# Optimization experiments

Hardware: AMD Instinct MI355X
Metric: run time of the kernel (lower is better)

## Reference

```python
import math
import jax, jax.numpy as jnp
import numpy as np

N_HEAD = 16

def rms_norm(x, w, eps=1e-6):
    x32 = x.astype(jnp.float32)
    ms = jnp.mean(x32 * x32, axis=-1, keepdims=True)
    y = (x32 * jax.lax.rsqrt(ms + eps)).astype(x.dtype)
    return y * w

def apply_rope(x, cos, sin):
    # x: [B,H,S,D], cos/sin: [S,D/2] broadcast over B,H
    half = x.shape[-1] // 2
    x1, x2 = x[..., :half], x[..., half:]
    return jnp.concatenate((x1 * cos - x2 * sin, x2 * cos + x1 * sin), axis=-1).astype(x.dtype)

def setup_inputs() -> dict:
    key = jax.random.key(0)
    ks = jax.random.split(key, 8)
    B, S, D = 1, 4096, 1024
    hd = D // N_HEAD
    x = jax.random.normal(ks[0], (B, S, D), dtype=jnp.float32)
    # rotary embeddings
    inv_freq = 1.0 / (10000.0 ** (jnp.arange(0, hd, 2, dtype=jnp.float32) / hd))  # [hd/2]
    ang = jnp.arange(S, dtype=jnp.float32)[:, None] * inv_freq  # [S, hd/2]
    cos, sin = jnp.cos(ang), jnp.sin(ang)
    # additive causal mask [1,1,S,S]
    causal = jnp.tril(jnp.ones((S, S), dtype=bool))
    attention_mask = jnp.where(causal, 0.0, -1e9).astype(jnp.float32)[None, None]
    init = 0.02
    wq = jax.random.normal(ks[1], (D, D), dtype=jnp.float32) * init
    wk = jax.random.normal(ks[2], (D, D), dtype=jnp.float32) * init
    wv = jax.random.normal(ks[3], (D, D), dtype=jnp.float32) * init
    wo = jax.random.normal(ks[4], (D, D), dtype=jnp.float32) * init
    q_norm_w = jnp.ones((hd,), dtype=jnp.float32)
    k_norm_w = jnp.ones((hd,), dtype=jnp.float32)
    return {"x": x, "cos": cos, "sin": sin, "attention_mask": attention_mask,
            "wq": wq, "wk": wk, "wv": wv, "wo": wo,
            "q_norm_w": q_norm_w, "k_norm_w": k_norm_w}

def reference(x, cos, sin, attention_mask, wq, wk, wv, wo, q_norm_w, k_norm_w):
    B, S, D = x.shape
    H = N_HEAD
    hd = D // H
    q = (x @ wq.T).reshape(B, S, H, hd)
    k = (x @ wk.T).reshape(B, S, H, hd)
    v = (x @ wv.T).reshape(B, S, H, hd)
    q = jnp.swapaxes(rms_norm(q, q_norm_w), 1, 2)  # [B,H,S,hd]
    k = jnp.swapaxes(rms_norm(k, k_norm_w), 1, 2)
    v = jnp.swapaxes(v, 1, 2)
    q = apply_rope(q, cos, sin)
    k = apply_rope(k, cos, sin)
    scores = jnp.einsum('bhqd,bhkd->bhqk', q, k) / math.sqrt(hd)
    scores = scores + attention_mask
    attn = jax.nn.softmax(scores.astype(jnp.float32), axis=-1).astype(q.dtype)
    o = jnp.einsum('bhqk,bhkd->bhqd', attn, v)  # [B,H,S,hd]
    o = jnp.swapaxes(o, 1, 2).reshape(B, S, D)
    return o @ wo.T
```

## Files before the change

### kernel.cpp

```cpp
#include <hip/hip_runtime.h>

#define S_LEN 4096
#define DIM   1024
#define NH    16
#define HD    64

typedef __bf16 bf16;
typedef __attribute__((ext_vector_type(8)))  __bf16 bf16x8;
typedef __attribute__((ext_vector_type(4)))  float  f32x4;
typedef __attribute__((ext_vector_type(16))) float  f32x16;
typedef __attribute__((ext_vector_type(4)))  unsigned int uint4v;

typedef __attribute__((address_space(3))) void lds_void;
typedef __attribute__((address_space(1))) void g_void;

#if __has_builtin(__builtin_amdgcn_exp2f)
#define EXP2(x) __builtin_amdgcn_exp2f(x)
#else
#define EXP2(x) exp2f(x)
#endif

__device__ __forceinline__ void gl_lds16(const void* g, void* l) {
    __builtin_amdgcn_global_load_lds((g_void*)(void*)g, (lds_void*)l, 16, 0, 0);
}

__device__ __forceinline__ unsigned int pk2(float a, float b) {
    unsigned short ua = __builtin_bit_cast(unsigned short, (bf16)a);
    unsigned short ub = __builtin_bit_cast(unsigned short, (bf16)b);
    return (unsigned int)ua | ((unsigned int)ub << 16);
}

__device__ __forceinline__ int ksw23(int x) {
    return (x & ~12) | ((x & 8) >> 1) | ((x & 4) << 1);
}

__global__ __launch_bounds__(256) void f2b_all(
    const float* __restrict__ x,  const float* __restrict__ wq,
    const float* __restrict__ wk, const float* __restrict__ wv,
    const float* __restrict__ wo,
    bf16* __restrict__ xb, bf16* __restrict__ wqkv, bf16* __restrict__ wob)
{
    int b = blockIdx.x;
    const float* src; bf16* dst; int base;
    if (b < 2048)      { src = x;  dst = xb;              base = b; }
    else if (b < 2560) { src = wq; dst = wqkv;            base = b - 2048; }
    else if (b < 3072) { src = wk; dst = wqkv + 1048576;  base = b - 2560; }
    else if (b < 3584) { src = wv; dst = wqkv + 2097152;  base = b - 3072; }
    else               { src = wo; dst = wob;             base = b - 3584; }
    int i = base * 2048 + threadIdx.x * 8;
    float4 a = *(const float4*)(src + i);
    float4 c = *(const float4*)(src + i + 4);
    bf16x8 r;
    r[0]=(bf16)a.x; r[1]=(bf16)a.y; r[2]=(bf16)a.z; r[3]=(bf16)a.w;
    r[4]=(bf16)c.x; r[5]=(bf16)c.y; r[6]=(bf16)c.z; r[7]=(bf16)c.w;
    *(bf16x8*)(dst + i) = r;
}

template <int MODE>
__global__ __launch_bounds__(256) void gemm_bt(
    const bf16* __restrict__ A, const bf16* __restrict__ B,
    int M, int N, int K,
    float* __restrict__ outF,
    bf16* __restrict__ outQ, bf16* __restrict__ outK, bf16* __restrict__ outV,
    const float* __restrict__ cosb, const float* __restrict__ sinb,
    const float* __restrict__ qw,   const float* __restrict__ kw)
{
    __shared__ bf16 As[128][32];
    __shared__ bf16 Bs[128][32];
    const int bm = blockIdx.x, bn = blockIdx.y;
    const int tid  = threadIdx.x;
    const int wave = tid >> 6, lane = tid & 63;
    const int g = lane >> 4, r = lane & 15;
    const int wr = wave >> 1, wc = wave & 1;
    const int rr = lane >> 2, cc = (lane & 3) * 8;

    f32x4 acc[4][4] = {};

    const bf16* Ab = A + (size_t)(bm * 128) * K;
    const bf16* Bb = B + (size_t)(bn * 128) * K;

    for (int k0 = 0; k0 < K; k0 += 32) {
        #pragma unroll
        for (int i = 0; i < 2; ++i) {
            gl_lds16(Ab + (size_t)(wave*32 + i*16 + rr) * K + k0 + cc, &As[wave*32 + i*16][0]);
            gl_lds16(Bb + (size_t)(wave*32 + i*16 + rr) * K + k0 + cc, &Bs[wave*32 + i*16][0]);
        }
        __syncthreads();
        bf16x8 a[4], b[4];
        #pragma unroll
        for (int m = 0; m < 4; ++m) a[m] = *(const bf16x8*)&As[wr*64 + m*16 + r][g*8];
        #pragma unroll
        for (int n = 0; n < 4; ++n) b[n] = *(const bf16x8*)&Bs[wc*64 + n*16 + r][g*8];
        #pragma unroll
        for (int m = 0; m < 4; ++m)
            #pragma unroll
            for (int n = 0; n < 4; ++n)
                acc[m][n] = __builtin_amdgcn_mfma_f32_16x16x32_bf16(a[m], b[n], acc[m][n], 0, 0, 0);
        __syncthreads();
    }

    if (MODE == 0) {
        #pragma unroll
        for (int m = 0; m < 4; ++m)
            #pragma unroll
            for (int n = 0; n < 4; ++n)
                #pragma unroll
                for (int i = 0; i < 4; ++i) {
                    int row = bm*128 + wr*64 + m*16 + g*4 + i;
                    int col = bn*128 + wc*64 + n*16 + r;
                    outF[(size_t)row * N + col] = acc[m][n][i];
                }
    } else if (bn >= 16) {
        #pragma unroll
        for (int m = 0; m < 4; ++m)
            #pragma unroll
            for (int n = 0; n < 4; ++n)
                #pragma unroll
                for (int i = 0; i < 4; ++i) {
                    int row = bm*128 + wr*64 + m*16 + g*4 + i;
                    int col = bn*128 + wc*64 + n*16 + r;
                    int c2 = col - 2048;
                    int hh = c2 >> 6, d = c2 & 63;
                    int pos = ksw23(row & 63) ^ ((d & 7) << 3);
                    outV[((size_t)(hh * HD + d)) * S_LEN + (row & ~63) + pos] = (bf16)acc[m][n][i];
                }
    } else {
        const bool isK = (bn >= 8);
        const float* wn = isK ? kw : qw;
        bf16* dst = isK ? outK : outQ;
        const int h = ((bn & 7) << 1) | wc;
        float wv4[4];
        #pragma unroll
        for (int n = 0; n < 4; ++n) wv4[n] = wn[n * 16 + r];
        #pragma unroll
        for (int m = 0; m < 4; ++m)
            #pragma unroll
            for (int i = 0; i < 4; ++i) {
                int srow = bm*128 + wr*64 + m*16 + g*4 + i;
                float ss = acc[m][0][i]*acc[m][0][i] + acc[m][1][i]*acc[m][1][i]
                         + acc[m][2][i]*acc[m][2][i] + acc[m][3][i]*acc[m][3][i];
                ss += __shfl_xor(ss, 1);
                ss += __shfl_xor(ss, 2);
                ss += __shfl_xor(ss, 4);
                ss += __shfl_xor(ss, 8);
                float rn = rsqrtf(ss * (1.0f / 64.0f) + 1e-6f);
                float xn0 = acc[m][0][i] * rn * wv4[0];
                float xn1 = acc[m][1][i] * rn * wv4[1];
                float xn2 = acc[m][2][i] * rn * wv4[2];
                float xn3 = acc[m][3][i] * rn * wv4[3];
                float c0 = cosb[srow * 32 + r],      c1 = cosb[srow * 32 + 16 + r];
                float s0 = sinb[srow * 32 + r],      s1 = sinb[srow * 32 + 16 + r];
                float y0 = xn0 * c0 - xn2 * s0;
                float y1 = xn1 * c1 - xn3 * s1;
                float y2 = xn2 * c0 + xn0 * s0;
                float y3 = xn3 * c1 + xn1 * s1;
                size_t ob = ((size_t)h * S_LEN + srow) * HD;
                if (isK) {
                    int sw = (srow & 7) << 3;
                    dst[ob + ((     r) ^ sw)] = (bf16)y0;
                    dst[ob + ((16 + r) ^ sw)] = (bf16)y1;
                    dst[ob + ((32 + r) ^ sw)] = (bf16)y2;
                    dst[ob + ((48 + r) ^ sw)] = (bf16)y3;
                } else {
                    dst[ob +      r] = (bf16)y0;
                    dst[ob + 16 + r] = (bf16)y1;
                    dst[ob + 32 + r] = (bf16)y2;
                    dst[ob + 48 + r] = (bf16)y3;
                }
            }
    }
}

__global__ __launch_bounds__(256, 4) void attn_kernel(
    const bf16* __restrict__ q, const bf16* __restrict__ k,
    const bf16* __restrict__ vt,
    bf16* __restrict__ Opc, float* __restrict__ lpc)
{
    __shared__ bf16 Ks[2][64][64];
    __shared__ bf16 Vt[2][64][64];

    const int idx = blockIdx.x;
    const int h = idx & 15;
    const int u = idx >> 4;
    const int qt = 31 - (u >> 2);
    const int c  = u & 3;
    const int nt = 2 * qt + 2;
    const int t0 = (c * nt) >> 2;
    const int t1 = ((c + 1) * nt) >> 2;

    const int q0 = qt * 128;
    const int tid = threadIdx.x;
    const int wave = tid >> 6, lane = tid & 63;
    const int l31 = lane & 31, hi = lane >> 5;

    const bf16* qh  = q  + (size_t)h * S_LEN * HD;
    const bf16* kh  = k  + (size_t)h * S_LEN * HD;
    const bf16* vth = vt + (size_t)h * HD * S_LEN;

    const int qrow = q0 + wave * 32 + l31;
    bf16x8 qf[4];
    #pragma unroll
    for (int ds4 = 0; ds4 < 4; ++ds4)
        qf[ds4] = *(const bf16x8*)(qh + (size_t)qrow * HD + ds4 * 16 + hi * 8);

    float l_run = 0.f;
    f32x16 acc_o[2] = {};

    const int srow = lane >> 3, scol = (lane & 7) * 8;
    const float C1 = 0.125f * 1.44269504088896f;
    const float C2 = 8.0f * 1.44269504088896f;

    auto stage = [&](int t, int buf) {
        const int k0 = t * 64;
        const bf16* kb = kh + (size_t)(k0 + wave * 16) * HD;
        gl_lds16(kb + (size_t)(srow    ) * HD + scol, &Ks[buf][wave * 16][0]);
        gl_lds16(kb + (size_t)(srow + 8) * HD + scol, &Ks[buf][wave * 16 + 8][0]);
        const bf16* vb = vth + (size_t)(wave * 16) * S_LEN + k0;
        gl_lds16(vb + (size_t)(srow    ) * S_LEN + scol, &Vt[buf][wave * 16][0]);
        gl_lds16(vb + (size_t)(srow + 8) * S_LEN + scol, &Vt[buf][wave * 16 + 8][0]);
    };

#define COMPUTE_TILE(T, BUF)                                                  \
    do {                                                                      \
        const int k0_ = (T) * 64;                                             \
        const bool masked_ = ((T) >= 2 * qt);                                 \
        f32x16 sacc_[2];                                                      \
        __builtin_amdgcn_s_setprio(1);                                        \
        _Pragma("unroll")                                                     \
        for (int kn = 0; kn < 2; ++kn) {                                      \
            const int krow = kn * 32 + l31;                                   \
            const int sw = (krow & 7) << 3;                                   \
            f32x16 z = {};                                                    \
            _Pragma("unroll")                                                 \
            for (int ds4 = 0; ds4 < 4; ++ds4) {                               \
                bf16x8 kfr = *(const bf16x8*)&Ks[BUF][krow][(ds4 * 16 + hi * 8) ^ sw]; \
                z = __builtin_amdgcn_mfma_f32_32x32x16_bf16(kfr, qf[ds4], z, 0, 0, 0); \
            }                                                                 \
            sacc_[kn] = z;                                                    \
        }                                                                     \
        __builtin_amdgcn_s_setprio(0);                                        \
        float p_[32];                                                         \
        _Pragma("unroll")                                                     \
        for (int kn = 0; kn < 2; ++kn)                                        \
            _Pragma("unroll")                                                 \
            for (int rg = 0; rg < 16; ++rg) {                                 \
                float e = EXP2(fmaf(sacc_[kn][rg], C1, -C2));                 \
                if (masked_) {                                                \
                    int kloc = kn * 32 + (rg & 3) + 8 * (rg >> 2) + 4 * hi;   \
                    if (k0_ + kloc > qrow) e = 0.f;                           \
                }                                                             \
                p_[kn * 16 + rg] = e;                                         \
            }                                                                 \
        float s0_ = 0.f, s1_ = 0.f, s2_ = 0.f, s3_ = 0.f;                     \
        _Pragma("unroll")                                                     \
        for (int j = 0; j < 8; ++j) {                                         \
            s0_ += p_[4*j];   s1_ += p_[4*j+1];                               \
            s2_ += p_[4*j+2]; s3_ += p_[4*j+3];                               \
        }                                                                     \
        float rs_ = (s0_ + s1_) + (s2_ + s3_);                                \
        rs_ += __shfl_xor(rs_, 32);                                           \
        l_run += rs_;                                                         \
        bf16x8 pa_[4];                                                        \
        _Pragma("unroll")                                                     \
        for (int ks4 = 0; ks4 < 4; ++ks4) {                                   \
            uint4v w_;                                                        \
            w_.x = pk2(p_[8*ks4+0], p_[8*ks4+1]);                             \
            w_.y = pk2(p_[8*ks4+2], p_[8*ks4+3]);                             \
            w_.z = pk2(p_[8*ks4+4], p_[8*ks4+5]);                             \
            w_.w = pk2(p_[8*ks4+6], p_[8*ks4+7]);                             \
            pa_[ks4] = __builtin_bit_cast(bf16x8, w_);                        \
        }                                                                     \
        __builtin_amdgcn_s_setprio(1);                                        \
        _Pragma("unroll")                                                     \
        for (int n = 0; n < 2; ++n) {                                         \
            const int d = n * 32 + l31;                                       \
            const int sw = (d & 7) << 3;                                      \
            f32x16 a = acc_o[n];                                              \
            _Pragma("unroll")                                                 \
            for (int ks4 = 0; ks4 < 4; ++ks4) {                               \
                bf16x8 vfr = *(const bf16x8*)&Vt[BUF][d][(ks4 * 16 + hi * 8) ^ sw]; \
                a = __builtin_amdgcn_mfma_f32_32x32x16_bf16(pa_[ks4], vfr, a, 0, 0, 0); \
            }                                                                 \
            acc_o[n] = a;                                                     \
        }                                                                     \
        __builtin_amdgcn_s_setprio(0);                                        \
    } while (0)

    if (t0 < t1) {
        stage(t0, 0);
        asm volatile("s_waitcnt vmcnt(0)" ::: "memory");
        __syncthreads();
        int t = t0;
        while (t + 2 <= t1) {
            stage(t + 1, 1);
            COMPUTE_TILE(t, 0);
            asm volatile("s_waitcnt vmcnt(0)" ::: "memory");
            __syncthreads();
            if (t + 2 < t1) stage(t + 2, 0);
            COMPUTE_TILE(t + 1, 1);
            asm volatile("s_waitcnt vmcnt(0)" ::: "memory");
            __syncthreads();
            t += 2;
        }
        if (t < t1) COMPUTE_TILE(t, 0);
    }
#undef COMPUTE_TILE

    bf16* Op = Opc + (size_t)c * S_LEN * DIM;
    #pragma unroll
    for (int n = 0; n < 2; ++n)
        #pragma unroll
        for (int rg = 0; rg < 16; ++rg) {
            int s_abs = q0 + wave * 32 + (rg & 3) + 8 * (rg >> 2) + 4 * hi;
            Op[(size_t)s_abs * DIM + h * HD + n * 32 + l31] = (bf16)acc_o[n][rg];
        }
    if (lane < 32)
        lpc[c * (NH * S_LEN) + h * S_LEN + (q0 + wave * 32 + lane)] = l_run;
}

__global__ __launch_bounds__(256) void combine_kernel(
    const bf16* __restrict__ Opc, const float* __restrict__ lpc,
    bf16* __restrict__ o)
{
    int gid = blockIdx.x * 256 + threadIdx.x;
    int e = gid * 8;
    int s = e >> 10, h = (e & 1023) >> 6;
    float a[8] = {};
    #pragma unroll
    for (int c = 0; c < 4; ++c) {
        bf16x8 v = *(const bf16x8*)(Opc + (size_t)c * S_LEN * DIM + e);
        #pragma unroll
        for (int j = 0; j < 8; ++j) a[j] += (float)v[j];
    }
    float l = 0.f;
    #pragma unroll
    for (int c = 0; c < 4; ++c) l += lpc[c * (NH * S_LEN) + h * S_LEN + s];
    float inv = __builtin_amdgcn_rcpf(l);
    bf16x8 rv;
    #pragma unroll
    for (int j = 0; j < 8; ++j) rv[j] = (bf16)(a[j] * inv);
    *(bf16x8*)(o + e) = rv;
}

extern "C" void kernel_launch(void* const* d_in, const int* in_sizes, int n_in,
                              void* d_out, int out_size, void* d_ws, size_t ws_size,
                              hipStream_t stream)
{
    const float* x    = (const float*)d_in[0];
    const float* cosb = (const float*)d_in[1];
    const float* sinb = (const float*)d_in[2];
    const float* wq   = (const float*)d_in[4];
    const float* wk   = (const float*)d_in[5];
    const float* wv   = (const float*)d_in[6];
    const float* wo   = (const float*)d_in[7];
    const float* qw   = (const float*)d_in[8];
    const float* kw   = (const float*)d_in[9];

    char* ws = (char*)d_ws;
    const size_t MB = 1024 * 1024;
    bf16*  wob   = (bf16*)(ws + 0);
    bf16*  q_ws  = (bf16*)(ws + 2 * MB);
    bf16*  k_ws  = (bf16*)(ws + 10 * MB);
    bf16*  vt_ws = (bf16*)(ws + 18 * MB);
    bf16*  Opc   = (bf16*)(ws + 26 * MB);
    bf16*  o_ws  = (bf16*)(ws + 26 * MB);
    bf16*  xb    = (bf16*)(ws + 26 * MB);
    bf16*  wqkv  = (bf16*)(ws + 34 * MB);
    float* lpc   = (float*)(ws + 58 * MB);

    f2b_all<<<4096, 256, 0, stream>>>(x, wq, wk, wv, wo, xb, wqkv, wob);

    gemm_bt<1><<<dim3(32, 24), 256, 0, stream>>>(xb, wqkv, 4096, 3072, 1024,
                                                 nullptr, q_ws, k_ws, vt_ws,
                                                 cosb, sinb, qw, kw);
    attn_kernel<<<2048, 256, 0, stream>>>(q_ws, k_ws, vt_ws, Opc, lpc);
    combine_kernel<<<4096 * 1024 / 8 / 256, 256, 0, stream>>>(Opc, lpc, o_ws);
    gemm_bt<0><<<dim3(32, 8), 256, 0, stream>>>(o_ws, wob, 4096, 1024, 1024,
                                                (float*)d_out, nullptr, nullptr, nullptr,
                                                nullptr, nullptr, nullptr, nullptr);
}
```

Before: 141.3 us.

## Replace QKV GEMM with 256x256 tile double-buffered pipelined kernel

The fused QKV projection GEMM moves from 128x128 tiles with 256 threads and a load-sync-compute loop to 256x256 tiles with 512 threads. Two LDS buffers with 64-wide K chunks let the global-to-LDS staging of the next chunk run under the current chunk's MFMAs, using split barriers, vmcnt waits and setprio. The goal is more data reuse per tile and hiding load latency. The trade-off is only 192 blocks, so one wave of blocks on a 256-CU part, plus a large register and LDS footprint at occupancy 1. The output GEMM is unchanged and is split into its own kernel.

```diff
diff --git a/kernel.cpp b/kernel.cpp
--- a/kernel.cpp
+++ b/kernel.cpp
@@ -56,107 +56,118 @@
     *(bf16x8*)(dst + i) = r;
 }
 
-template <int MODE>
-__global__ __launch_bounds__(256) void gemm_bt(
+__global__ __launch_bounds__(512, 1) void qkv256(
     const bf16* __restrict__ A, const bf16* __restrict__ B,
-    int M, int N, int K,
-    float* __restrict__ outF,
     bf16* __restrict__ outQ, bf16* __restrict__ outK, bf16* __restrict__ outV,
     const float* __restrict__ cosb, const float* __restrict__ sinb,
     const float* __restrict__ qw,   const float* __restrict__ kw)
 {
-    __shared__ bf16 As[128][32];
-    __shared__ bf16 Bs[128][32];
+    __shared__ bf16 LA[2][256][64];
+    __shared__ bf16 LB[2][256][64];
     const int bm = blockIdx.x, bn = blockIdx.y;
     const int tid  = threadIdx.x;
     const int wave = tid >> 6, lane = tid & 63;
-    const int g = lane >> 4, r = lane & 15;
-    const int wr = wave >> 1, wc = wave & 1;
-    const int rr = lane >> 2, cc = (lane & 3) * 8;
-
-    f32x4 acc[4][4] = {};
-
-    const bf16* Ab = A + (size_t)(bm * 128) * K;
-    const bf16* Bb = B + (size_t)(bn * 128) * K;
-
-    for (int k0 = 0; k0 < K; k0 += 32) {
-        #pragma unroll
-        for (int i = 0; i < 2; ++i) {
-            gl_lds16(Ab + (size_t)(wave*32 + i*16 + rr) * K + k0 + cc, &As[wave*32 + i*16][0]);
-            gl_lds16(Bb + (size_t)(wave*32 + i*16 + rr) * K + k0 + cc, &Bs[wave*32 + i*16][0]);
-        }
-        __syncthreads();
-        bf16x8 a[4], b[4];
-        #pragma unroll
-        for (int m = 0; m < 4; ++m) a[m] = *(const bf16x8*)&As[wr*64 + m*16 + r][g*8];
-        #pragma unroll
-        for (int n = 0; n < 4; ++n) b[n] = *(const bf16x8*)&Bs[wc*64 + n*16 + r][g*8];
-        #pragma unroll
-        for (int m = 0; m < 4; ++m)
-            #pragma unroll
-            for (int n = 0; n < 4; ++n)
-                acc[m][n] = __builtin_amdgcn_mfma_f32_16x16x32_bf16(a[m], b[n], acc[m][n], 0, 0, 0);
-        __syncthreads();
+    const int r = lane & 15, g = lane >> 4;
+    const int wm = wave >> 2, wn = wave & 3;
+    const int K = 1024;
+
+    const bf16* aBase = A + (size_t)(bm * 256 + (tid >> 3)) * K + (lane & 7) * 8;
+    const bf16* bBase = B + (size_t)(bn * 256 + (tid >> 3)) * K + (lane & 7) * 8;
+
+    f32x4 acc[8][4] = {};
+    bf16x8 bq[4];
+
+#define STG_A(BUF, MH, KT) do {                                               \
+    gl_lds16(aBase + (size_t)(MH) * 131072 + (KT) * 64,                       \
+             &LA[BUF][(MH) * 128 + wave * 8][0]);                             \
+    gl_lds16(aBase + (size_t)(MH) * 131072 + 65536 + (KT) * 64,               \
+             &LA[BUF][(MH) * 128 + 64 + wave * 8][0]);                        \
+} while (0)
+
+#define STG_B(BUF, MH, KT) do {                                               \
+    gl_lds16(bBase + (size_t)(MH) * 131072 + (KT) * 64,                       \
+             &LB[BUF][(MH) * 128 + wave * 8][0]);                             \
+    gl_lds16(bBase + (size_t)(MH) * 131072 + 65536 + (KT) * 64,               \
+             &LB[BUF][(MH) * 128 + 64 + wave * 8][0]);                        \
+} while (0)
+
+#define PHASE(BUF, KC, MH, DOB, STG, VM, TRAIL) do {                          \
+    STG;                                                                      \
+    if (VM) asm volatile("s_waitcnt vmcnt(2)" ::: "memory");                  \
+    __builtin_amdgcn_s_barrier();                                             \
+    if (DOB) {                                                                \
+        _Pragma("unroll")                                                     \
+        for (int nr = 0; nr < 4; ++nr)                                        \
+            bq[nr] = *(const bf16x8*)&LB[BUF][wn * 64 + nr * 16 + r][(KC) * 32 + g * 8]; \
+    }                                                                         \
+    bf16x8 af[4];                                                             \
+    _Pragma("unroll")                                                         \
+    for (int mr = 0; mr < 4; ++mr)                                            \
+        af[mr] = *(const bf16x8*)&LA[BUF][wm * 128 + (MH) * 64 + mr * 16 + r][(KC) * 32 + g * 8]; \
+    __builtin_amdgcn_s_setprio(1);                                            \
+    _Pragma("unroll")                                                         \
+    for (int mr = 0; mr < 4; ++mr)                                            \
+        _Pragma("unroll")                                                     \
+        for (int nr = 0; nr < 4; ++nr)                                        \
+            acc[(MH) * 4 + mr][nr] = __builtin_amdgcn_mfma_f32_16x16x32_bf16( \
+                af[mr], bq[nr], acc[(MH) * 4 + mr][nr], 0, 0, 0);             \
+    __builtin_amdgcn_s_setprio(0);                                            \
+    if (TRAIL) __builtin_amdgcn_s_barrier();                                  \
+} while (0)
+
+    STG_A(0, 0, 0); STG_A(0, 1, 0); STG_B(0, 0, 0); STG_B(0, 1, 0);
+
+    for (int it = 0; it < 8; ++it) {
+        const int k1 = 2 * it + 1;
+        const int k2 = (2 * it + 2) & 15;
+        PHASE(0, 0, 0, 1, STG_A(1, 0, k1), 1, 0);
+        PHASE(0, 0, 1, 0, STG_A(1, 1, k1), 0, 0);
+        PHASE(0, 1, 0, 1, STG_B(1, 0, k1), 0, 0);
+        PHASE(0, 1, 1, 0, STG_B(1, 1, k1), 0, 1);
+        PHASE(1, 0, 0, 1, STG_A(0, 0, k2), 1, 0);
+        PHASE(1, 0, 1, 0, STG_A(0, 1, k2), 0, 0);
+        PHASE(1, 1, 0, 1, STG_B(0, 0, k2), 0, 0);
+        PHASE(1, 1, 1, 0, STG_B(0, 1, k2), 0, 1);
     }
-
-    if (MODE == 0) {
-        #pragma unroll
-        for (int m = 0; m < 4; ++m)
-            #pragma unroll
-            for (int n = 0; n < 4; ++n)
-                #pragma unroll
-                for (int i = 0; i < 4; ++i) {
-                    int row = bm*128 + wr*64 + m*16 + g*4 + i;
-                    int col = bn*128 + wc*64 + n*16 + r;
-                    outF[(size_t)row * N + col] = acc[m][n][i];
-                }
-    } else if (bn >= 16) {
-        #pragma unroll
-        for (int m = 0; m < 4; ++m)
-            #pragma unroll
-            for (int n = 0; n < 4; ++n)
-                #pragma unroll
-                for (int i = 0; i < 4; ++i) {
-                    int row = bm*128 + wr*64 + m*16 + g*4 + i;
-                    int col = bn*128 + wc*64 + n*16 + r;
-                    int c2 = col - 2048;
-                    int hh = c2 >> 6, d = c2 & 63;
-                    int pos = ksw23(row & 63) ^ ((d & 7) << 3);
-                    outV[((size_t)(hh * HD + d)) * S_LEN + (row & ~63) + pos] = (bf16)acc[m][n][i];
-                }
-    } else {
-        const bool isK = (bn >= 8);
-        const float* wn = isK ? kw : qw;
+    asm volatile("s_waitcnt vmcnt(0)" ::: "memory");
+#undef PHASE
+#undef STG_A
+#undef STG_B
+
+    if (bn < 8) {
+        const bool isK = (bn >= 4);
+        const float* wvp = isK ? kw : qw;
         bf16* dst = isK ? outK : outQ;
-        const int h = ((bn & 7) << 1) | wc;
+        const int h = (bn & 3) * 4 + wn;
         float wv4[4];
         #pragma unroll
-        for (int n = 0; n < 4; ++n) wv4[n] = wn[n * 16 + r];
-        #pragma unroll
-        for (int m = 0; m < 4; ++m)
+        for (int nr = 0; nr < 4; ++nr) wv4[nr] = wvp[nr * 16 + r];
+        #pragma unroll
+        for (int mg = 0; mg < 8; ++mg)
             #pragma unroll
             for (int i = 0; i < 4; ++i) {
-                int srow = bm*128 + wr*64 + m*16 + g*4 + i;
-                float ss = acc[m][0][i]*acc[m][0][i] + acc[m][1][i]*acc[m][1][i]
-                         + acc[m][2][i]*acc[m][2][i] + acc[m][3][i]*acc[m][3][i];
+                int s = bm * 256 + wm * 128 + mg * 16 + g * 4 + i;
+                float a0 = acc[mg][0][i], a1 = acc[mg][1][i];
+                float a2 = acc[mg][2][i], a3 = acc[mg][3][i];
+                float ss = a0 * a0 + a1 * a1 + a2 * a2 + a3 * a3;
                 ss += __shfl_xor(ss, 1);
                 ss += __shfl_xor(ss, 2);
                 ss += __shfl_xor(ss, 4);
                 ss += __shfl_xor(ss, 8);
                 float rn = rsqrtf(ss * (1.0f / 64.0f) + 1e-6f);
-                float xn0 = acc[m][0][i] * rn * wv4[0];
-                float xn1 = acc[m][1][i] * rn * wv4[1];
-                float xn2 = acc[m][2][i] * rn * wv4[2];
-                float xn3 = acc[m][3][i] * rn * wv4[3];
-                float c0 = cosb[srow * 32 + r],      c1 = cosb[srow * 32 + 16 + r];
-                float s0 = sinb[srow * 32 + r],      s1 = sinb[srow * 32 + 16 + r];
+                float xn0 = a0 * rn * wv4[0];
+                float xn1 = a1 * rn * wv4[1];
+                float xn2 = a2 * rn * wv4[2];
+                float xn3 = a3 * rn * wv4[3];
+                float c0 = cosb[s * 32 + r],      c1 = cosb[s * 32 + 16 + r];
+                float s0 = sinb[s * 32 + r],      s1 = sinb[s * 32 + 16 + r];
                 float y0 = xn0 * c0 - xn2 * s0;
                 float y1 = xn1 * c1 - xn3 * s1;
                 float y2 = xn2 * c0 + xn0 * s0;
                 float y3 = xn3 * c1 + xn1 * s1;
-                size_t ob = ((size_t)h * S_LEN + srow) * HD;
+                size_t ob = ((size_t)h * S_LEN + s) * HD;
                 if (isK) {
-                    int sw = (srow & 7) << 3;
+                    int sw = (s & 7) << 3;
                     dst[ob + ((     r) ^ sw)] = (bf16)y0;
                     dst[ob + ((16 + r) ^ sw)] = (bf16)y1;
                     dst[ob + ((32 + r) ^ sw)] = (bf16)y2;
@@ -168,7 +179,71 @@
                     dst[ob + 48 + r] = (bf16)y3;
                 }
             }
+    } else {
+        const int hh = (bn - 8) * 4 + wn;
+        #pragma unroll
+        for (int mg = 0; mg < 8; ++mg)
+            #pragma unroll
+            for (int nr = 0; nr < 4; ++nr)
+                #pragma unroll
+                for (int i = 0; i < 4; ++i) {
+                    int row = bm * 256 + wm * 128 + mg * 16 + g * 4 + i;
+                    int d = nr * 16 + r;
+                    int pos = ksw23(row & 63) ^ ((d & 7) << 3);
+                    outV[((size_t)(hh * HD + d)) * S_LEN + (row & ~63) + pos] =
+                        (bf16)acc[mg][nr][i];
+                }
     }
+}
+
+__global__ __launch_bounds__(256) void gemm_out(
+    const bf16* __restrict__ A, const bf16* __restrict__ B,
+    int M, int N, int K, float* __restrict__ outF)
+{
+    __shared__ bf16 As[128][32];
+    __shared__ bf16 Bs[128][32];
+    const int bm = blockIdx.x, bn = blockIdx.y;
+    const int tid  = threadIdx.x;
+    const int wave = tid >> 6, lane = tid & 63;
+    const int g = lane >> 4, r = lane & 15;
+    const int wr = wave >> 1, wc = wave & 1;
+    const int rr = lane >> 2, cc = (lane & 3) * 8;
+
+    f32x4 acc[4][4] = {};
+
+    const bf16* Ab = A + (size_t)(bm * 128) * K;
+    const bf16* Bb = B + (size_t)(bn * 128) * K;
+
+    for (int k0 = 0; k0 < K; k0 += 32) {
+        #pragma unroll
+        for (int i = 0; i < 2; ++i) {
+            gl_lds16(Ab + (size_t)(wave*32 + i*16 + rr) * K + k0 + cc, &As[wave*32 + i*16][0]);
+            gl_lds16(Bb + (size_t)(wave*32 + i*16 + rr) * K + k0 + cc, &Bs[wave*32 + i*16][0]);
+        }
+        __syncthreads();
+        bf16x8 a[4], b[4];
+        #pragma unroll
+        for (int m = 0; m < 4; ++m) a[m] = *(const bf16x8*)&As[wr*64 + m*16 + r][g*8];
+        #pragma unroll
+        for (int n = 0; n < 4; ++n) b[n] = *(const bf16x8*)&Bs[wc*64 + n*16 + r][g*8];
+        #pragma unroll
+        for (int m = 0; m < 4; ++m)
+            #pragma unroll
+            for (int n = 0; n < 4; ++n)
+                acc[m][n] = __builtin_amdgcn_mfma_f32_16x16x32_bf16(a[m], b[n], acc[m][n], 0, 0, 0);
+        __syncthreads();
+    }
+
+    #pragma unroll
+    for (int m = 0; m < 4; ++m)
+        #pragma unroll
+        for (int n = 0; n < 4; ++n)
+            #pragma unroll
+            for (int i = 0; i < 4; ++i) {
+                int row = bm*128 + wr*64 + m*16 + g*4 + i;
+                int col = bn*128 + wc*64 + n*16 + r;
+                outF[(size_t)row * N + col] = acc[m][n][i];
+            }
 }
 
 __global__ __launch_bounds__(256, 4) void attn_kernel(
@@ -370,12 +445,10 @@
 
     f2b_all<<<4096, 256, 0, stream>>>(x, wq, wk, wv, wo, xb, wqkv, wob);
 
-    gemm_bt<1><<<dim3(32, 24), 256, 0, stream>>>(xb, wqkv, 4096, 3072, 1024,
-                                                 nullptr, q_ws, k_ws, vt_ws,
-                                                 cosb, sinb, qw, kw);
+    qkv256<<<dim3(16, 12), 512, 0, stream>>>(xb, wqkv, q_ws, k_ws, vt_ws,
+                                             cosb, sinb, qw, kw);
     attn_kernel<<<2048, 256, 0, stream>>>(q_ws, k_ws, vt_ws, Opc, lpc);
     combine_kernel<<<4096 * 1024 / 8 / 256, 256, 0, stream>>>(Opc, lpc, o_ws);
-    gemm_bt<0><<<dim3(32, 8), 256, 0, stream>>>(o_ws, wob, 4096, 1024, 1024,
-                                                (float*)d_out, nullptr, nullptr, nullptr,
-                                                nullptr, nullptr, nullptr, nullptr);
-}
+    gemm_out<<<dim3(32, 8), 256, 0, stream>>>(o_ws, wob, 4096, 1024, 1024,
+                                              (float*)d_out);
+}
```

New measurement: 154.4 us. 9.3% more time.
